# Kernel optimization log

Measured on AMD Instinct MI355X. Metric: run time of the kernel, lower is better.

The kernel has to match this reference:

```python
import jax, jax.numpy as jnp
import numpy as np

N_NODES = 50000
N_EDGES = 800000
D_IN = 96
D_OUT = 96


def setup_inputs() -> dict:
    key = jax.random.key(0)
    k1, k2, k3, k4, k5, k6 = jax.random.split(key, 6)
    x = jax.random.normal(k1, (N_NODES, D_IN), dtype=jnp.float32)
    edge_index = jax.random.randint(k2, (2, N_EDGES), 0, N_NODES, dtype=jnp.int32)
    W_lin = jax.random.normal(k3, (D_OUT, D_IN), dtype=jnp.float32) * 0.1
    b_lin = jax.random.normal(k4, (D_OUT,), dtype=jnp.float32) * 0.1
    W_root = jax.random.normal(k5, (D_OUT, D_IN), dtype=jnp.float32) * 0.1
    b_root = jax.random.normal(k6, (D_OUT,), dtype=jnp.float32) * 0.1
    return {"x": x, "edge_index": edge_index, "W_lin": W_lin, "b_lin": b_lin,
            "W_root": W_root, "b_root": b_root}


def reference(x, edge_index, W_lin, b_lin, W_root, b_root):
    # GCNConv with separate root weight: out = relu(scatter_add(norm * lin(x_src), dst) + root(x))
    src, dst = edge_index[0], edge_index[1]
    n = x.shape[0]
    # symmetric degree normalization (in-degree based, clamped to avoid div0)
    deg = jax.ops.segment_sum(jnp.ones(src.shape[0], dtype=x.dtype), dst, num_segments=n)
    dinv = jax.lax.rsqrt(jnp.maximum(deg, 1.0))
    norm = dinv[src] * dinv[dst]                      # [E]
    h = x @ W_lin.T + b_lin                           # [N, D_OUT] neighbor transform
    msgs = h[src] * norm[:, None]                     # [E, D_OUT] gathered + scaled
    agg = jax.ops.segment_sum(msgs, dst, num_segments=n)  # scatter-add
    out = agg + x @ W_root.T + b_root                 # root/self contribution
    return jax.nn.relu(out)
```

## Files before the change

kernel.cpp:

```cpp
#include <hip/hip_runtime.h>

#define D 96
#define BSH 5
#define SCAP 1088
#define SBSH 8
#define NSBMAX 224
#define SBCAP 4608
#define CH 2048

typedef __attribute__((ext_vector_type(8))) short bf16x8;
typedef __attribute__((ext_vector_type(4))) float f32x4;

__device__ __forceinline__ unsigned bf16_rne(float f) {
    unsigned u = __float_as_uint(f);
    return (u + 0x7fffu + ((u >> 16) & 1u)) >> 16;
}
__device__ __forceinline__ float blo(unsigned u) { return __uint_as_float(u << 16); }
__device__ __forceinline__ float bhi(unsigned u) { return __uint_as_float(u & 0xffff0000u); }

__global__ __launch_bounds__(512) void bin_kernel(
    const int* __restrict__ ei, int* __restrict__ scur, unsigned* __restrict__ sp,
    const float* __restrict__ Wlin, const float* __restrict__ Wroot,
    unsigned* __restrict__ wfrag, int E, int NSB)
{
    __shared__ int hist[NSBMAX];
    __shared__ int lstart[NSBMAX];
    __shared__ int gbase[NSBMAX];
    __shared__ unsigned stage[CH];
    int t = threadIdx.x;
    int gt = blockIdx.x * 512 + t;
    int e0 = blockIdx.x * CH;
    int ne = min(CH, E - e0);
    for (int i = t; i < NSB; i += 512) hist[i] = 0;
    if (gt < 9216) {
        int f = gt >> 8, r = gt & 255;
        int l = r >> 2, jp = r & 3;
        int ct = f / 6, st = f % 6;
        int nn = ct * 16 + (l & 15);
        int k  = st * 32 + (l >> 4) * 8 + jp * 2;
        const float* W = (k < D) ? Wlin : Wroot;
        int kk = (k < D) ? k : k - D;
        float v0 = W[nn * D + kk], v1 = W[nn * D + kk + 1];
        wfrag[gt] = bf16_rne(v0) | (bf16_rne(v1) << 16);
    }
    __syncthreads();
    unsigned pk[4]; int bk[4];
    int base = e0 + t * 4;
    if (base + 3 < E) {
        int4 a = *(const int4*)(ei + base);
        int4 b = *(const int4*)(ei + E + base);
        pk[0] = (unsigned)a.x | ((unsigned)b.x << 16); bk[0] = b.x >> SBSH;
        pk[1] = (unsigned)a.y | ((unsigned)b.y << 16); bk[1] = b.y >> SBSH;
        pk[2] = (unsigned)a.z | ((unsigned)b.z << 16); bk[2] = b.z >> SBSH;
        pk[3] = (unsigned)a.w | ((unsigned)b.w << 16); bk[3] = b.w >> SBSH;
    } else {
        #pragma unroll
        for (int u = 0; u < 4; ++u) {
            int e = base + u;
            if (e < E) { pk[u] = (unsigned)ei[e] | ((unsigned)ei[E + e] << 16); bk[u] = ei[E + e] >> SBSH; }
            else bk[u] = -1;
        }
    }
    #pragma unroll
    for (int u = 0; u < 4; ++u)
        if (bk[u] >= 0) atomicAdd(&hist[bk[u]], 1);
    __syncthreads();
    if (t < 64) {
        int carry = 0;
        for (int c0 = 0; c0 < NSB; c0 += 64) {
            int i = c0 + t;
            int v = (i < NSB) ? hist[i] : 0;
            int incl = v;
            #pragma unroll
            for (int d = 1; d < 64; d <<= 1) {
                int uu = __shfl_up(incl, d, 64);
                if (t >= d) incl += uu;
            }
            if (i < NSB) lstart[i] = carry + incl - v;
            carry += __shfl(incl, 63, 64);
        }
    }
    __syncthreads();
    for (int i = t; i < NSB; i += 512) {
        int c = hist[i];
        if (c > 0) gbase[i] = atomicAdd(&scur[i], c);
        hist[i] = lstart[i];
    }
    __syncthreads();
    #pragma unroll
    for (int u = 0; u < 4; ++u) {
        if (bk[u] >= 0) {
            int p = atomicAdd(&hist[bk[u]], 1);
            stage[p] = pk[u];
        }
    }
    __syncthreads();
    for (int i = t; i < ne; i += 512) {
        unsigned w = stage[i];
        int sb = (int)(w >> (16 + SBSH));
        int slot = gbase[sb] + (i - lstart[sb]);
        if (slot < SBCAP) sp[(size_t)sb * SBCAP + slot] = w;
    }
}

__global__ __launch_bounds__(256) void xspack_kernel(
    const float* __restrict__ x, unsigned* __restrict__ xs, int n)
{
    int gt = blockIdx.x * 256 + threadIdx.x;
    int gsz = gridDim.x * 256;
    int ntask = (n + 1) * 24;
    for (int i = gt; i < ntask; i += gsz) {
        int row = i / 24, q = i - row * 24;
        uint2 o;
        if (row < n) {
            float4 v = ((const float4*)x)[(size_t)row * 24 + q];
            o.x = bf16_rne(v.x) | (bf16_rne(v.y) << 16);
            o.y = bf16_rne(v.z) | (bf16_rne(v.w) << 16);
        } else { o.x = 0u; o.y = 0u; }
        *(uint2*)(xs + (size_t)row * 48 + q * 2) = o;
    }
}

__global__ __launch_bounds__(512) void dinv_kernel(
    const int* __restrict__ scur, const unsigned* __restrict__ sp,
    float* __restrict__ dinv, int n)
{
    __shared__ int hist[256];
    int t = threadIdx.x;
    if (t < 256) hist[t] = 0;
    __syncthreads();
    int ne = min(scur[blockIdx.x], SBCAP);
    const unsigned* spb = sp + (size_t)blockIdx.x * SBCAP;
    for (int i0 = t * 4; i0 < ne; i0 += 2048) {
        if (i0 + 3 < ne) {
            uint4 w = *(const uint4*)(spb + i0);
            atomicAdd(&hist[(w.x >> 16) & 255], 1);
            atomicAdd(&hist[(w.y >> 16) & 255], 1);
            atomicAdd(&hist[(w.z >> 16) & 255], 1);
            atomicAdd(&hist[(w.w >> 16) & 255], 1);
        } else {
            for (int i = i0; i < ne; ++i) atomicAdd(&hist[(spb[i] >> 16) & 255], 1);
        }
    }
    __syncthreads();
    if (t < 256) {
        int node = (blockIdx.x << SBSH) + t;
        if (node < n) {
            int d = hist[t];
            dinv[node] = rsqrtf((float)(d > 1 ? d : 1));
        }
    }
    if (blockIdx.x == 0 && t == 256) dinv[n] = 0.f;
}

__global__ __launch_bounds__(256, 8) void bgather_gemm_kernel(
    const int* __restrict__ scur, const unsigned* __restrict__ sp,
    const float* __restrict__ dinv, const unsigned* __restrict__ xs,
    const unsigned* __restrict__ wfrag, const float* __restrict__ blin,
    const float* __restrict__ broot, float* __restrict__ out, int n)
{
    __shared__ uint2 sd[SCAP];
    __shared__ int hist[32];
    __shared__ int seg[33];
    __shared__ int cur[32];
    __shared__ int pq;
    __shared__ unsigned yt[32][52];
    __shared__ float sv32[32];
    int t = threadIdx.x;
    int nwg = gridDim.x;
    int qq = nwg >> 3, rr = nwg & 7;
    int xcd = blockIdx.x & 7, ix = blockIdx.x >> 3;
    int bid = (xcd < rr ? xcd * (qq + 1) : rr * (qq + 1) + (xcd - rr) * qq) + ix;
    int node0 = bid << BSH;
    int sb = bid >> 3;
    int lb = bid & 7;
    int ne = min(scur[sb], SBCAP);
    const unsigned* spb = sp + (size_t)sb * SBCAP;
    const unsigned ZR = (unsigned)n;
    if (t < 32) hist[t] = 0;
    if (t < 8) sd[t] = make_uint2(ZR, 0u);
    __syncthreads();
    for (int i0 = t * 4; i0 < ne; i0 += 1024) {
        if (i0 + 3 < ne) {
            uint4 w4 = *(const uint4*)(spb + i0);
            if (((w4.x >> (16 + BSH)) & 7) == (unsigned)lb) atomicAdd(&hist[(w4.x >> 16) & 31], 1);
            if (((w4.y >> (16 + BSH)) & 7) == (unsigned)lb) atomicAdd(&hist[(w4.y >> 16) & 31], 1);
            if (((w4.z >> (16 + BSH)) & 7) == (unsigned)lb) atomicAdd(&hist[(w4.z >> 16) & 31], 1);
            if (((w4.w >> (16 + BSH)) & 7) == (unsigned)lb) atomicAdd(&hist[(w4.w >> 16) & 31], 1);
        } else {
            for (int i = i0; i < ne; ++i) {
                unsigned w = spb[i];
                if (((w >> (16 + BSH)) & 7) == (unsigned)lb) atomicAdd(&hist[(w >> 16) & 31], 1);
            }
        }
    }
    __syncthreads();
    if (t == 0) {
        int run = 8;
        #pragma unroll
        for (int i = 0; i < 32; ++i) {
            seg[i] = run;
            run += (hist[i] + 7) & ~7;
            if (run > SCAP) run = SCAP;
        }
        seg[32] = run;
        pq = 0;
    }
    __syncthreads();
    if (t < 32) cur[t] = seg[t];
    __syncthreads();
    for (int i0 = t * 4; i0 < ne; i0 += 1024) {
        if (i0 + 3 < ne) {
            uint4 w4 = *(const uint4*)(spb + i0);
            if (((w4.x >> (16 + BSH)) & 7) == (unsigned)lb) { int p = atomicAdd(&cur[(w4.x >> 16) & 31], 1); if (p < SCAP) sd[p].x = w4.x & 0xffffu; }
            if (((w4.y >> (16 + BSH)) & 7) == (unsigned)lb) { int p = atomicAdd(&cur[(w4.y >> 16) & 31], 1); if (p < SCAP) sd[p].x = w4.y & 0xffffu; }
            if (((w4.z >> (16 + BSH)) & 7) == (unsigned)lb) { int p = atomicAdd(&cur[(w4.z >> 16) & 31], 1); if (p < SCAP) sd[p].x = w4.z & 0xffffu; }
            if (((w4.w >> (16 + BSH)) & 7) == (unsigned)lb) { int p = atomicAdd(&cur[(w4.w >> 16) & 31], 1); if (p < SCAP) sd[p].x = w4.w & 0xffffu; }
        } else {
            for (int i = i0; i < ne; ++i) {
                unsigned w = spb[i];
                if (((w >> (16 + BSH)) & 7) == (unsigned)lb) { int p = atomicAdd(&cur[(w >> 16) & 31], 1); if (p < SCAP) sd[p].x = w & 0xffffu; }
            }
        }
    }
    __syncthreads();
    if (t < 32) {
        int e = seg[t + 1];
        int s = seg[t] + hist[t]; if (s > e) s = e;
        for (int p2 = s; p2 < e; ++p2) sd[p2] = make_uint2(ZR, 0u);
    }
    __syncthreads();
    int tot = seg[32];
    for (int i = t; i < tot; i += 256) sd[i].y = __float_as_uint(dinv[sd[i].x]);
    __syncthreads();

    int l = t & 63;
    int g = l / 12;
    int m = l - g * 12;
    unsigned loff = (unsigned)(m << 4);
    const char* xb = (const char*)xs;

    for (;;) {
        int p;
        if (l == 0) p = atomicAdd(&pq, 1);
        p = __builtin_amdgcn_readfirstlane(p);
        if (p >= 16) break;
        int ndA = p * 2, ndB = ndA + 1;
        int jsA = seg[ndA], itA = (seg[ndA + 1] - jsA) >> 3;
        int jsB = seg[ndB], itB = (seg[ndB + 1] - jsB) >> 3;
        int iters = itA > itB ? itA : itB;
        float aA0=0.f,aA1=0.f,aA2=0.f,aA3=0.f,aA4=0.f,aA5=0.f,aA6=0.f,aA7=0.f;
        float aB0=0.f,aB1=0.f,aB2=0.f,aB3=0.f,aB4=0.f,aB5=0.f,aB6=0.f,aB7=0.f;
        float sn = 0.f;
        for (int it = 0; it < iters; ++it) {
            int baseA = (it < itA) ? (jsA + it * 8) : 0;
            int baseB = (it < itB) ? (jsB + it * 8) : 0;
            if (l < 48) {
                uint2 qA0 = sd[baseA + g], qA1 = sd[baseA + 4 + g];
                uint2 qB0 = sd[baseB + g], qB1 = sd[baseB + 4 + g];
                uint4 vA0 = *(const uint4*)(xb + qA0.x * 192u + loff);
                uint4 vA1 = *(const uint4*)(xb + qA1.x * 192u + loff);
                uint4 vB0 = *(const uint4*)(xb + qB0.x * 192u + loff);
                uint4 vB1 = *(const uint4*)(xb + qB1.x * 192u + loff);
                float dA0 = __uint_as_float(qA0.y), dA1 = __uint_as_float(qA1.y);
                float dB0 = __uint_as_float(qB0.y), dB1 = __uint_as_float(qB1.y);
                aA0 += dA0 * blo(vA0.x); aA1 += dA0 * bhi(vA0.x); aA2 += dA0 * blo(vA0.y); aA3 += dA0 * bhi(vA0.y);
                aA4 += dA0 * blo(vA0.z); aA5 += dA0 * bhi(vA0.z); aA6 += dA0 * blo(vA0.w); aA7 += dA0 * bhi(vA0.w);
                aA0 += dA1 * blo(vA1.x); aA1 += dA1 * bhi(vA1.x); aA2 += dA1 * blo(vA1.y); aA3 += dA1 * bhi(vA1.y);
                aA4 += dA1 * blo(vA1.z); aA5 += dA1 * bhi(vA1.z); aA6 += dA1 * blo(vA1.w); aA7 += dA1 * bhi(vA1.w);
                aB0 += dB0 * blo(vB0.x); aB1 += dB0 * bhi(vB0.x); aB2 += dB0 * blo(vB0.y); aB3 += dB0 * bhi(vB0.y);
                aB4 += dB0 * blo(vB0.z); aB5 += dB0 * bhi(vB0.z); aB6 += dB0 * blo(vB0.w); aB7 += dB0 * bhi(vB0.w);
                aB0 += dB1 * blo(vB1.x); aB1 += dB1 * bhi(vB1.x); aB2 += dB1 * blo(vB1.y); aB3 += dB1 * bhi(vB1.y);
                aB4 += dB1 * blo(vB1.z); aB5 += dB1 * bhi(vB1.z); aB6 += dB1 * blo(vB1.w); aB7 += dB1 * bhi(vB1.w);
            } else {
                int bs = (l < 56) ? baseA : baseB;
                sn += __uint_as_float(sd[bs + (l & 7)].y);
            }
        }
        float stA = 0.f, stB = 0.f;
        #pragma unroll
        for (int u = 0; u < 8; ++u) {
            stA += __shfl(sn, 48 + u, 64);
            stB += __shfl(sn, 56 + u, 64);
        }
        int l24 = (l + 24) & 63, l12 = (l + 12) & 63;
        aA0 += __shfl(aA0, l24, 64); aA1 += __shfl(aA1, l24, 64); aA2 += __shfl(aA2, l24, 64); aA3 += __shfl(aA3, l24, 64);
        aA4 += __shfl(aA4, l24, 64); aA5 += __shfl(aA5, l24, 64); aA6 += __shfl(aA6, l24, 64); aA7 += __shfl(aA7, l24, 64);
        aB0 += __shfl(aB0, l24, 64); aB1 += __shfl(aB1, l24, 64); aB2 += __shfl(aB2, l24, 64); aB3 += __shfl(aB3, l24, 64);
        aB4 += __shfl(aB4, l24, 64); aB5 += __shfl(aB5, l24, 64); aB6 += __shfl(aB6, l24, 64); aB7 += __shfl(aB7, l24, 64);
        aA0 += __shfl(aA0, l12, 64); aA1 += __shfl(aA1, l12, 64); aA2 += __shfl(aA2, l12, 64); aA3 += __shfl(aA3, l12, 64);
        aA4 += __shfl(aA4, l12, 64); aA5 += __shfl(aA5, l12, 64); aA6 += __shfl(aA6, l12, 64); aA7 += __shfl(aA7, l12, 64);
        aB0 += __shfl(aB0, l12, 64); aB1 += __shfl(aB1, l12, 64); aB2 += __shfl(aB2, l12, 64); aB3 += __shfl(aB3, l12, 64);
        aB4 += __shfl(aB4, l12, 64); aB5 += __shfl(aB5, l12, 64); aB6 += __shfl(aB6, l12, 64); aB7 += __shfl(aB7, l12, 64);
        int nodeA = node0 + ndA, nodeB = node0 + ndB;
        float dnA = (nodeA < n) ? dinv[nodeA] : 0.f;
        float dnB = (nodeB < n) ? dinv[nodeB] : 0.f;
        if (l < 12) {
            uint4 oA, oB;
            oA.x = bf16_rne(dnA * aA0) | (bf16_rne(dnA * aA1) << 16);
            oA.y = bf16_rne(dnA * aA2) | (bf16_rne(dnA * aA3) << 16);
            oA.z = bf16_rne(dnA * aA4) | (bf16_rne(dnA * aA5) << 16);
            oA.w = bf16_rne(dnA * aA6) | (bf16_rne(dnA * aA7) << 16);
            oB.x = bf16_rne(dnB * aB0) | (bf16_rne(dnB * aB1) << 16);
            oB.y = bf16_rne(dnB * aB2) | (bf16_rne(dnB * aB3) << 16);
            oB.z = bf16_rne(dnB * aB4) | (bf16_rne(dnB * aB5) << 16);
            oB.w = bf16_rne(dnB * aB6) | (bf16_rne(dnB * aB7) << 16);
            *(uint4*)&yt[ndA][4 * m] = oA;
            *(uint4*)&yt[ndB][4 * m] = oB;
        } else if (l == 48) {
            sv32[ndA] = dnA * stA;
            sv32[ndB] = dnB * stB;
        }
    }
    __syncthreads();

    int wv = t >> 6;
    int lane15 = l & 15, quad = l >> 4;
    for (int j = wv; j < 12; j += 4) {
        int rg = j / 6, ct = j % 6;
        int r0 = node0 + rg * 16;
        f32x4 accY = (f32x4){0.f, 0.f, 0.f, 0.f};
        f32x4 accX = (f32x4){0.f, 0.f, 0.f, 0.f};
        #pragma unroll
        for (int st_ = 0; st_ < 3; ++st_) {
            bf16x8 a = *(const bf16x8*)(&yt[rg * 16 + lane15][st_ * 16 + quad * 4]);
            bf16x8 b = *(const bf16x8*)(wfrag + ((ct * 6 + st_) * 64 + l) * 4);
            accY = __builtin_amdgcn_mfma_f32_16x16x32_bf16(a, b, accY, 0, 0, 0);
        }
        int ar = r0 + lane15;
        #pragma unroll
        for (int sm = 0; sm < 3; ++sm) {
            bf16x8 a = (bf16x8){0, 0, 0, 0, 0, 0, 0, 0};
            if (ar < n) a = *(const bf16x8*)(xs + (size_t)ar * 48 + sm * 16 + quad * 4);
            bf16x8 b = *(const bf16x8*)(wfrag + ((ct * 6 + 3 + sm) * 64 + l) * 4);
            accX = __builtin_amdgcn_mfma_f32_16x16x32_bf16(a, b, accX, 0, 0, 0);
        }
        int col = ct * 16 + lane15;
        float blc = blin[col], brc = broot[col];
        #pragma unroll
        for (int reg = 0; reg < 4; ++reg) {
            int r = r0 + quad * 4 + reg;
            if (r < n) {
                float sv = sv32[rg * 16 + quad * 4 + reg];
                float v = accY[reg] + accX[reg] + sv * blc + brc;
                out[(size_t)r * D + col] = fmaxf(v, 0.f);
            }
        }
    }
}

extern "C" void kernel_launch(void* const* d_in, const int* in_sizes, int n_in,
                              void* d_out, int out_size, void* d_ws, size_t ws_size,
                              hipStream_t stream) {
    const float* x     = (const float*)d_in[0];
    const int*   ei    = (const int*)d_in[1];
    const float* Wlin  = (const float*)d_in[2];
    const float* blin  = (const float*)d_in[3];
    const float* Wroot = (const float*)d_in[4];
    const float* broot = (const float*)d_in[5];
    float* out = (float*)d_out;

    const int n = in_sizes[0] / D;
    const int E = in_sizes[1] / 2;
    const int NB = (n + 31) >> BSH;
    const int NSB = (n + 255) >> SBSH;

    int*      scur  = (int*)d_ws;
    float*    dinv  = (float*)(scur + 256);
    unsigned* sp    = (unsigned*)(dinv + n + 4);
    unsigned* wfrag = sp + (size_t)NSB * SBCAP;
    unsigned* xs    = wfrag + 9216;

    hipMemsetAsync(scur, 0, 256 * sizeof(int), stream);

    bin_kernel<<<(E + CH - 1) / CH, 512, 0, stream>>>(ei, scur, sp, Wlin, Wroot,
                                                      wfrag, E, NSB);
    xspack_kernel<<<1024, 256, 0, stream>>>(x, xs, n);
    dinv_kernel<<<NSB, 512, 0, stream>>>(scur, sp, dinv, n);
    bgather_gemm_kernel<<<NB, 256, 0, stream>>>(scur, sp, dinv, xs, wfrag,
                                                blin, broot, out, n);
}
```

Baseline: 141.2 us.

## Fuse degree counting and x packing into bin kernel, drop dinv kernel

Global atomic in-degree counting and bf16 packing of x move into the edge-binning kernel, which removes the separate xspack and dinv launches. The gather-GEMM kernel now reads per-node degree directly instead of rescanning its superbucket to build a local histogram, and computes rsqrt on the fly. This cuts two kernel launches and a redundant pass over the binned edges. In exchange it adds 800k global atomics, a larger memset, and a lower occupancy hint (7 instead of 8).

Measured after the change: 164.4 us. 16.5% more time.

```diff
diff --git a/kernel.cpp b/kernel.cpp
--- a/kernel.cpp
+++ b/kernel.cpp
@@ -18,10 +18,12 @@
 __device__ __forceinline__ float blo(unsigned u) { return __uint_as_float(u << 16); }
 __device__ __forceinline__ float bhi(unsigned u) { return __uint_as_float(u & 0xffff0000u); }
 
-__global__ __launch_bounds__(512) void bin_kernel(
+__global__ __launch_bounds__(512) void prep_kernel(
     const int* __restrict__ ei, int* __restrict__ scur, unsigned* __restrict__ sp,
-    const float* __restrict__ Wlin, const float* __restrict__ Wroot,
-    unsigned* __restrict__ wfrag, int E, int NSB)
+    int* __restrict__ deg, const float* __restrict__ Wlin,
+    const float* __restrict__ Wroot, unsigned* __restrict__ wfrag,
+    const float* __restrict__ x, unsigned* __restrict__ xs,
+    int E, int NSB, int n)
 {
     __shared__ int hist[NSBMAX];
     __shared__ int lstart[NSBMAX];
@@ -53,12 +55,19 @@
         pk[1] = (unsigned)a.y | ((unsigned)b.y << 16); bk[1] = b.y >> SBSH;
         pk[2] = (unsigned)a.z | ((unsigned)b.z << 16); bk[2] = b.z >> SBSH;
         pk[3] = (unsigned)a.w | ((unsigned)b.w << 16); bk[3] = b.w >> SBSH;
+        atomicAdd(&deg[b.x], 1);
+        atomicAdd(&deg[b.y], 1);
+        atomicAdd(&deg[b.z], 1);
+        atomicAdd(&deg[b.w], 1);
     } else {
         #pragma unroll
         for (int u = 0; u < 4; ++u) {
             int e = base + u;
-            if (e < E) { pk[u] = (unsigned)ei[e] | ((unsigned)ei[E + e] << 16); bk[u] = ei[E + e] >> SBSH; }
-            else bk[u] = -1;
+            if (e < E) {
+                int dd = ei[E + e];
+                pk[u] = (unsigned)ei[e] | ((unsigned)dd << 16); bk[u] = dd >> SBSH;
+                atomicAdd(&deg[dd], 1);
+            } else bk[u] = -1;
         }
     }
     #pragma unroll
@@ -101,13 +110,7 @@
         int slot = gbase[sb] + (i - lstart[sb]);
         if (slot < SBCAP) sp[(size_t)sb * SBCAP + slot] = w;
     }
-}
-
-__global__ __launch_bounds__(256) void xspack_kernel(
-    const float* __restrict__ x, unsigned* __restrict__ xs, int n)
-{
-    int gt = blockIdx.x * 256 + threadIdx.x;
-    int gsz = gridDim.x * 256;
+    int gsz = gridDim.x * 512;
     int ntask = (n + 1) * 24;
     for (int i = gt; i < ntask; i += gsz) {
         int row = i / 24, q = i - row * 24;
@@ -121,46 +124,14 @@
     }
 }
 
-__global__ __launch_bounds__(512) void dinv_kernel(
+__global__ __launch_bounds__(256, 7) void bgather_gemm_kernel(
     const int* __restrict__ scur, const unsigned* __restrict__ sp,
-    float* __restrict__ dinv, int n)
-{
-    __shared__ int hist[256];
-    int t = threadIdx.x;
-    if (t < 256) hist[t] = 0;
-    __syncthreads();
-    int ne = min(scur[blockIdx.x], SBCAP);
-    const unsigned* spb = sp + (size_t)blockIdx.x * SBCAP;
-    for (int i0 = t * 4; i0 < ne; i0 += 2048) {
-        if (i0 + 3 < ne) {
-            uint4 w = *(const uint4*)(spb + i0);
-            atomicAdd(&hist[(w.x >> 16) & 255], 1);
-            atomicAdd(&hist[(w.y >> 16) & 255], 1);
-            atomicAdd(&hist[(w.z >> 16) & 255], 1);
-            atomicAdd(&hist[(w.w >> 16) & 255], 1);
-        } else {
-            for (int i = i0; i < ne; ++i) atomicAdd(&hist[(spb[i] >> 16) & 255], 1);
-        }
-    }
-    __syncthreads();
-    if (t < 256) {
-        int node = (blockIdx.x << SBSH) + t;
-        if (node < n) {
-            int d = hist[t];
-            dinv[node] = rsqrtf((float)(d > 1 ? d : 1));
-        }
-    }
-    if (blockIdx.x == 0 && t == 256) dinv[n] = 0.f;
-}
-
-__global__ __launch_bounds__(256, 8) void bgather_gemm_kernel(
-    const int* __restrict__ scur, const unsigned* __restrict__ sp,
-    const float* __restrict__ dinv, const unsigned* __restrict__ xs,
+    const int* __restrict__ deg, const unsigned* __restrict__ xs,
     const unsigned* __restrict__ wfrag, const float* __restrict__ blin,
     const float* __restrict__ broot, float* __restrict__ out, int n)
 {
     __shared__ uint2 sd[SCAP];
-    __shared__ int hist[32];
+    __shared__ int histC[32];
     __shared__ int seg[33];
     __shared__ int cur[32];
     __shared__ int pq;
@@ -177,30 +148,18 @@
     int ne = min(scur[sb], SBCAP);
     const unsigned* spb = sp + (size_t)sb * SBCAP;
     const unsigned ZR = (unsigned)n;
-    if (t < 32) hist[t] = 0;
-    if (t < 8) sd[t] = make_uint2(ZR, 0u);
-    __syncthreads();
-    for (int i0 = t * 4; i0 < ne; i0 += 1024) {
-        if (i0 + 3 < ne) {
-            uint4 w4 = *(const uint4*)(spb + i0);
-            if (((w4.x >> (16 + BSH)) & 7) == (unsigned)lb) atomicAdd(&hist[(w4.x >> 16) & 31], 1);
-            if (((w4.y >> (16 + BSH)) & 7) == (unsigned)lb) atomicAdd(&hist[(w4.y >> 16) & 31], 1);
-            if (((w4.z >> (16 + BSH)) & 7) == (unsigned)lb) atomicAdd(&hist[(w4.z >> 16) & 31], 1);
-            if (((w4.w >> (16 + BSH)) & 7) == (unsigned)lb) atomicAdd(&hist[(w4.w >> 16) & 31], 1);
-        } else {
-            for (int i = i0; i < ne; ++i) {
-                unsigned w = spb[i];
-                if (((w >> (16 + BSH)) & 7) == (unsigned)lb) atomicAdd(&hist[(w >> 16) & 31], 1);
-            }
-        }
-    }
+    if (t < 32) {
+        int node = node0 + t;
+        histC[t] = (node < n) ? deg[node] : 0;
+    }
+    if (t >= 32 && t < 40) sd[t - 32] = make_uint2(ZR, 0u);
     __syncthreads();
     if (t == 0) {
         int run = 8;
         #pragma unroll
         for (int i = 0; i < 32; ++i) {
             seg[i] = run;
-            run += (hist[i] + 7) & ~7;
+            run += (histC[i] + 7) & ~7;
             if (run > SCAP) run = SCAP;
         }
         seg[32] = run;
@@ -226,12 +185,20 @@
     __syncthreads();
     if (t < 32) {
         int e = seg[t + 1];
-        int s = seg[t] + hist[t]; if (s > e) s = e;
+        int s = seg[t] + histC[t]; if (s > e) s = e;
         for (int p2 = s; p2 < e; ++p2) sd[p2] = make_uint2(ZR, 0u);
     }
     __syncthreads();
     int tot = seg[32];
-    for (int i = t; i < tot; i += 256) sd[i].y = __float_as_uint(dinv[sd[i].x]);
+    for (int i = t; i < tot; i += 256) {
+        unsigned idx = sd[i].x;
+        float y = 0.f;
+        if (idx != ZR) {
+            int d = deg[idx];
+            y = rsqrtf((float)(d > 1 ? d : 1));
+        }
+        sd[i].y = __float_as_uint(y);
+    }
     __syncthreads();
 
     int l = t & 63;
@@ -293,8 +260,8 @@
         aB0 += __shfl(aB0, l12, 64); aB1 += __shfl(aB1, l12, 64); aB2 += __shfl(aB2, l12, 64); aB3 += __shfl(aB3, l12, 64);
         aB4 += __shfl(aB4, l12, 64); aB5 += __shfl(aB5, l12, 64); aB6 += __shfl(aB6, l12, 64); aB7 += __shfl(aB7, l12, 64);
         int nodeA = node0 + ndA, nodeB = node0 + ndB;
-        float dnA = (nodeA < n) ? dinv[nodeA] : 0.f;
-        float dnB = (nodeB < n) ? dinv[nodeB] : 0.f;
+        float dnA = (nodeA < n) ? rsqrtf((float)(histC[ndA] > 1 ? histC[ndA] : 1)) : 0.f;
+        float dnB = (nodeB < n) ? rsqrtf((float)(histC[ndB] > 1 ? histC[ndB] : 1)) : 0.f;
         if (l < 12) {
             uint4 oA, oB;
             oA.x = bf16_rne(dnA * aA0) | (bf16_rne(dnA * aA1) << 16);
@@ -364,19 +331,18 @@
     const int E = in_sizes[1] / 2;
     const int NB = (n + 31) >> BSH;
     const int NSB = (n + 255) >> SBSH;
+    const int NBLK = (E + CH - 1) / CH;
 
     int*      scur  = (int*)d_ws;
-    float*    dinv  = (float*)(scur + 256);
-    unsigned* sp    = (unsigned*)(dinv + n + 4);
+    int*      deg   = (int*)(scur + 256);
+    unsigned* sp    = (unsigned*)(deg + n + 4);
     unsigned* wfrag = sp + (size_t)NSB * SBCAP;
     unsigned* xs    = wfrag + 9216;
 
-    hipMemsetAsync(scur, 0, 256 * sizeof(int), stream);
-
-    bin_kernel<<<(E + CH - 1) / CH, 512, 0, stream>>>(ei, scur, sp, Wlin, Wroot,
-                                                      wfrag, E, NSB);
-    xspack_kernel<<<1024, 256, 0, stream>>>(x, xs, n);
-    dinv_kernel<<<NSB, 512, 0, stream>>>(scur, sp, dinv, n);
-    bgather_gemm_kernel<<<NB, 256, 0, stream>>>(scur, sp, dinv, xs, wfrag,
+    hipMemsetAsync(scur, 0, (256 + n + 4) * sizeof(int), stream);
+
+    prep_kernel<<<NBLK, 512, 0, stream>>>(ei, scur, sp, deg, Wlin, Wroot,
+                                          wfrag, x, xs, E, NSB, n);
+    bgather_gemm_kernel<<<NB, 256, 0, stream>>>(scur, sp, deg, xs, wfrag,
                                                 blin, broot, out, n);
 }
```
